# Kernel tuning notes

Measured on AMD Instinct MI355X. Metric: run time of the kernel, lower is better.

## Reference

```python
import jax, jax.numpy as jnp
import numpy as np

DG = 8   # deformable groups
K = 3    # DCNv2 kernel size


def conv1x1(x, w):
    return jnp.einsum('bhwc,cf->bhwf', x, w)


def conv3x3_same(x, w, b):
    out = jax.lax.conv_general_dilated(x, w, (1, 1), 'SAME',
                                       dimension_numbers=('NHWC', 'HWIO', 'NHWC'))
    return out + b


def dcn_v2(x, offset, mask, weight, bias):
    # x: [B,H,W,C]; offset: [B,H,W,DG,K*K,2] (dy,dx); mask: [B,H,W,DG,K*K]
    B, H, W, C = x.shape
    cpg = C // DG
    ky, kx = jnp.meshgrid(jnp.arange(K) - (K // 2), jnp.arange(K) - (K // 2), indexing='ij')
    ky = ky.reshape(-1).astype(x.dtype)  # [K*K]
    kx = kx.reshape(-1).astype(x.dtype)
    iy = jnp.arange(H, dtype=x.dtype)[None, :, None, None, None]
    ix = jnp.arange(W, dtype=x.dtype)[None, None, :, None, None]
    yp = iy + ky + offset[..., 0]   # [B,H,W,DG,KK] sample rows
    xp = ix + kx + offset[..., 1]   # sample cols

    # group-major flattened feature map for gather: [B,DG,H*W,cpg]
    xt = jnp.transpose(x.reshape(B, H, W, DG, cpg), (0, 3, 1, 2, 4)).reshape(B, DG, H * W, cpg)

    def gather(yi, xi):
        valid = ((yi >= 0) & (yi < H) & (xi >= 0) & (xi < W)).astype(x.dtype)
        yc = jnp.clip(yi, 0, H - 1)
        xc = jnp.clip(xi, 0, W - 1)
        flat = (yc * W + xc).astype(jnp.int32)               # [B,H,W,DG,KK]
        idx = jnp.transpose(flat, (0, 3, 1, 2, 4)).reshape(B, DG, -1)
        v = jnp.take_along_axis(xt, idx[..., None], axis=2)  # [B,DG,H*W*KK,cpg]
        v = v.reshape(B, DG, H, W, K * K, cpg)
        v = jnp.transpose(v, (0, 2, 3, 1, 4, 5))             # [B,H,W,DG,KK,cpg]
        return v * valid[..., None]

    y0 = jnp.floor(yp); x0 = jnp.floor(xp)
    wy = (yp - y0)[..., None]; wx = (xp - x0)[..., None]
    val = (gather(y0, x0) * (1 - wy) * (1 - wx)
           + gather(y0, x0 + 1) * (1 - wy) * wx
           + gather(y0 + 1, x0) * wy * (1 - wx)
           + gather(y0 + 1, x0 + 1) * wy * wx)
    val = val * mask[..., None]                               # modulated sampling
    # [B,H,W,DG,KK,cpg] -> [B,H,W,KK,C] (global channel = g*cpg + r)
    val = jnp.transpose(val, (0, 1, 2, 4, 3, 5)).reshape(B, H, W, K * K, C)
    out = jnp.einsum('bhwkc,kcf->bhwf', val, weight.reshape(K * K, C, -1))
    return out + bias


def setup_inputs() -> dict:
    key = jax.random.key(0)
    ks = jax.random.split(key, 8)
    B, H, W, Cf, Cc, F = 4, 64, 64, 256, 256, 256
    fine = jax.random.normal(ks[0], (B, H, W, Cf), jnp.float32)
    coarse = jax.random.normal(ks[1], (B, H // 2, W // 2, Cc), jnp.float32)
    attend_w = jax.random.normal(ks[2], (Cf, Cf), jnp.float32) * 0.05
    select_w = jax.random.normal(ks[3], (Cf, F), jnp.float32) * 0.05
    offset_w = jax.random.normal(ks[4], (F + Cc, 2 * F), jnp.float32) * 0.05
    om_w = jax.random.normal(ks[5], (3, 3, 2 * F, DG * 3 * K * K), jnp.float32) * 0.01
    om_b = jnp.zeros((DG * 3 * K * K,), jnp.float32)
    dcn_w = jax.random.normal(ks[6], (3, 3, Cc, F), jnp.float32) * 0.05
    dcn_b = jnp.zeros((F,), jnp.float32)
    return {'fine': fine, 'coarse': coarse, 'attend_w': attend_w, 'select_w': select_w,
            'offset_w': offset_w, 'om_w': om_w, 'om_b': om_b, 'dcn_w': dcn_w, 'dcn_b': dcn_b}


def reference(fine, coarse, attend_w, select_w, offset_w, om_w, om_b, dcn_w, dcn_b):
    B, H, W, Cf = fine.shape
    Cc = coarse.shape[-1]
    # BilinearInterpolation: upsample coarse to fine resolution
    coarse_up = jax.image.resize(coarse, (B, H, W, Cc), 'bilinear')
    # FeatureSelection: GAP -> 1x1 sigmoid attention, residual gate, 1x1 proj
    attn = jax.nn.sigmoid(conv1x1(jnp.mean(fine, axis=(1, 2), keepdims=True), attend_w))
    fine_cal = conv1x1(fine * (attn + 1.0), select_w)
    # offset features from concat(selected fine, 2*coarse)
    align = conv1x1(jnp.concatenate([fine_cal, coarse_up * 2.0], axis=-1), offset_w)
    # DCNv2 internal offset/mask conv (3x3) on alignment features
    om = conv3x3_same(align, om_w, om_b)          # [B,H,W,DG*3*K*K]
    n_off = DG * 2 * K * K
    off = om[..., :n_off].reshape(B, H, W, DG, K * K, 2)
    mask = jax.nn.sigmoid(om[..., n_off:]).reshape(B, H, W, DG, K * K)
    aligned = dcn_v2(coarse_up, off, mask, dcn_w, dcn_b)
    return jax.nn.relu(aligned) + fine_cal
```

## Files before the change

kernel.cpp:

```cpp
#include <hip/hip_runtime.h>
#include <math.h>


typedef __attribute__((ext_vector_type(8))) short bf16x8;
typedef __attribute__((ext_vector_type(4))) short bf16x4;
typedef __attribute__((ext_vector_type(4))) float f32x4;
#define MFMA16(a,b,c) __builtin_amdgcn_mfma_f32_16x16x32_bf16(a,b,c,0,0,0)

__device__ inline short f2b(float x){
  union { float f; unsigned u; } v; v.f = x;
  unsigned r = v.u + 0x7FFFu + ((v.u >> 16) & 1u);
  return (short)(r >> 16);
}
__device__ inline float b2f(short s){
  union { unsigned u; float f; } v;
  v.u = ((unsigned)(unsigned short)s) << 16;
  return v.f;
}

#define OFS_GATE  1024u
#define OFS_PART  2048u
#define OFS_CUPB  264192u
#define OFS_FCAL  4458496u
#define OFS_ALGB  8652800u
#define OFS_OM    12847104u
#define OFS_DWB   16386048u
#define OFS_OMWB  16680960u
#define OFS_SWB   17270784u
#define OFS_OWB   17401856u

__global__ __launch_bounds__(256) void k_gap(const float* __restrict__ fine,
                                             float* __restrict__ part){
  __shared__ float red[4*256];
  int b = blockIdx.x >> 6, chunk = blockIdx.x & 63;
  int c4 = threadIdx.x & 63, rl = threadIdx.x >> 6;
  const float4* F4 = (const float4*)fine;
  float4 s = {0.f,0.f,0.f,0.f};
  for (int it = 0; it < 16; ++it){
    int row = chunk*64 + it*4 + rl;
    float4 v = F4[((size_t)(b*4096 + row))*64 + c4];
    s.x += v.x; s.y += v.y; s.z += v.z; s.w += v.w;
  }
  *(float4*)&red[rl*256 + c4*4] = s;
  __syncthreads();
  int c = threadIdx.x;
  part[(size_t)blockIdx.x*256 + c] = red[c] + red[256+c] + red[512+c] + red[768+c];
}

__global__ __launch_bounds__(256) void k_misc(const float* __restrict__ part,
                                              const float* __restrict__ aw,
                                              float* __restrict__ gate,
                                              const float* __restrict__ dw,
                                              const float* __restrict__ omw,
                                              const float* __restrict__ ow,
                                              const float* __restrict__ sw,
                                              short* __restrict__ dwb,
                                              short* __restrict__ omwb,
                                              short* __restrict__ owb,
                                              short* __restrict__ swb,
                                              const float* __restrict__ coarse,
                                              short* __restrict__ cupb){
  int blk = blockIdx.x;
  if (blk < 4){
    __shared__ float m[256];
    int b = blk, f = threadIdx.x;
    float sm = 0.f;
    for (int ch = 0; ch < 64; ++ch) sm += part[(size_t)(b*64 + ch)*256 + f];
    m[f] = sm * (1.f/4096.f);
    __syncthreads();
    float s = 0.f;
    for (int c = 0; c < 256; ++c) s += m[c] * aw[c*256 + f];
    gate[b*256 + f] = 1.f + 1.f/(1.f + expf(-s));
  } else if (blk < 292){
    int t = (blk - 4)*256 + threadIdx.x;
    int l = t & 63, nt = (t >> 6) & 15, ksg = t >> 10;
    int n = nt*16 + (l & 15);
    int kb = ksg*32 + (l >> 4)*8;
    bf16x8 o;
#pragma unroll
    for (int j = 0; j < 8; ++j) o[j] = f2b(dw[(size_t)(kb + j)*256 + n]);
    ((bf16x8*)dwb)[t] = o;
  } else if (blk < 868){
    int t = (blk - 292)*256 + threadIdx.x;
    int l = t & 63, nt = (t >> 6) & 15, ksg = t >> 10;
    int n = nt*16 + (l & 15);
    int kb = ksg*32 + (l >> 4)*8;
    bf16x8 o;
#pragma unroll
    for (int j = 0; j < 8; ++j)
      o[j] = (n < 216) ? f2b(omw[(size_t)(kb + j)*216 + n]) : (short)0;
    ((bf16x8*)omwb)[t] = o;
  } else if (blk < 996){
    int t = (blk - 868)*256 + threadIdx.x;
    int l = t & 63, nt = (t >> 6) & 31, ksg = t >> 11;
    int n = nt*16 + (l & 15);
    int kb = ksg*32 + (l >> 4)*8;
    float sc = (kb >= 256) ? 2.f : 1.f;
    bf16x8 o;
#pragma unroll
    for (int j = 0; j < 8; ++j) o[j] = f2b(sc * ow[(size_t)(kb + j)*512 + n]);
    ((bf16x8*)owb)[t] = o;
  } else if (blk < 1124){
    int t = (blk - 996)*256 + threadIdx.x;
    int l = t & 63, nt = (t >> 6) & 15, ksg = t >> 10;
    int n = nt*16 + (l & 15);
    int kb = ksg*32 + (l >> 4)*8;
    bf16x8 o;
#pragma unroll
    for (int j = 0; j < 8; ++j) o[j] = f2b(sw[(size_t)(kb + j)*256 + n]);
    ((bf16x8*)swb)[t] = o;
  } else {
    int idx = (blk - 1124)*256 + threadIdx.x;
    int c4 = idx & 63, x = (idx >> 6) & 63, y = (idx >> 12) & 63, b = idx >> 18;
    float fy = 0.5f*y - 0.25f, fx = 0.5f*x - 0.25f;
    float yf = floorf(fy), xf = floorf(fx);
    float wy = fy - yf, wx = fx - xf;
    int r0 = max(0, min(31, (int)yf)), r1 = max(0, min(31, (int)yf + 1));
    int c0 = max(0, min(31, (int)xf)), c1 = max(0, min(31, (int)xf + 1));
    const float4* src = (const float4*)coarse;
    float4 v00 = src[((b*32 + r0)*32 + c0)*64 + c4];
    float4 v01 = src[((b*32 + r0)*32 + c1)*64 + c4];
    float4 v10 = src[((b*32 + r1)*32 + c0)*64 + c4];
    float4 v11 = src[((b*32 + r1)*32 + c1)*64 + c4];
    float w00 = (1.f-wy)*(1.f-wx), w01 = (1.f-wy)*wx, w10 = wy*(1.f-wx), w11 = wy*wx;
    bf16x4 o = { f2b(v00.x*w00 + v01.x*w01 + v10.x*w10 + v11.x*w11),
                 f2b(v00.y*w00 + v01.y*w01 + v10.y*w10 + v11.y*w11),
                 f2b(v00.z*w00 + v01.z*w01 + v10.z*w10 + v11.z*w11),
                 f2b(v00.w*w00 + v01.w*w01 + v10.w*w10 + v11.w*w11) };
    ((bf16x4*)cupb)[idx] = o;
  }
}

#define FST 264
__global__ __launch_bounds__(512) void k_fa(const float* __restrict__ fine,
                                            const float* __restrict__ gate,
                                            const short* __restrict__ swb,
                                            const short* __restrict__ owb,
                                            const short* __restrict__ cupb,
                                            float* __restrict__ fcal,
                                            short* __restrict__ algb){
  __shared__ float g4[256];
  __shared__ short ab[32*FST];
  int bid = ((blockIdx.x & 7) << 6) | (blockIdx.x >> 3);
  int m0 = bid*32, b = m0 >> 12;
  int tid = threadIdx.x, lane = tid & 63, wave = tid >> 6;
  int arow = lane & 15, aquad = lane >> 4;
  if (tid < 256) g4[tid] = gate[b*256 + tid];
  __syncthreads();
  const float4* F4 = (const float4*)(fine + (size_t)m0*256);
  const float4* G4 = (const float4*)g4;
  for (int it = 0; it < 4; ++it){
    int idx = it*512 + tid;
    int row = idx >> 6, c4 = idx & 63;
    float4 v = F4[row*64 + c4];
    float4 gg = G4[c4];
    bf16x4 s4 = { f2b(v.x*gg.x), f2b(v.y*gg.y), f2b(v.z*gg.z), f2b(v.w*gg.w) };
    *(bf16x4*)&ab[row*FST + c4*4] = s4;
  }
  __syncthreads();
  f32x4 acc[2][2];
#pragma unroll
  for (int s = 0; s < 2; ++s)
#pragma unroll
    for (int t = 0; t < 2; ++t) acc[s][t] = (f32x4){0.f,0.f,0.f,0.f};
  const bf16x8* W8 = (const bf16x8*)swb;
  for (int ks = 0; ks < 8; ++ks){
    bf16x8 a0 = *(const bf16x8*)&ab[arow*FST + ks*32 + aquad*8];
    bf16x8 a1 = *(const bf16x8*)&ab[(16 + arow)*FST + ks*32 + aquad*8];
    const bf16x8* wp = W8 + ((size_t)(ks*16 + wave*2))*64 + lane;
#pragma unroll
    for (int t = 0; t < 2; ++t){
      bf16x8 bw = wp[t*64];
      acc[0][t] = MFMA16(a0, bw, acc[0][t]);
      acc[1][t] = MFMA16(a1, bw, acc[1][t]);
    }
  }
  __syncthreads();
#pragma unroll
  for (int t = 0; t < 2; ++t){
    int f = wave*32 + t*16 + arow;
#pragma unroll
    for (int s = 0; s < 2; ++s)
#pragma unroll
      for (int r = 0; r < 4; ++r){
        int mloc = s*16 + aquad*4 + r;
        float v = acc[s][t][r];
        fcal[(size_t)(m0 + mloc)*256 + f] = v;
        ab[mloc*FST + f] = f2b(v);
      }
  }
  __syncthreads();
  f32x4 acc2[2][4];
#pragma unroll
  for (int s = 0; s < 2; ++s)
#pragma unroll
    for (int t = 0; t < 4; ++t) acc2[s][t] = (f32x4){0.f,0.f,0.f,0.f};
  const bf16x8* OW8 = (const bf16x8*)owb;
  for (int ks = 0; ks < 16; ++ks){
    bf16x8 a0, a1;
    if (ks < 8){
      a0 = *(const bf16x8*)&ab[arow*FST + ks*32 + aquad*8];
      a1 = *(const bf16x8*)&ab[(16 + arow)*FST + ks*32 + aquad*8];
    } else {
      int ko = (ks - 8)*32 + aquad*8;
      a0 = *(const bf16x8*)(cupb + (size_t)(m0 + arow)*256 + ko);
      a1 = *(const bf16x8*)(cupb + (size_t)(m0 + 16 + arow)*256 + ko);
    }
    const bf16x8* wp = OW8 + ((size_t)(ks*32 + wave*4))*64 + lane;
#pragma unroll
    for (int t = 0; t < 4; ++t){
      bf16x8 bw = wp[t*64];
      acc2[0][t] = MFMA16(a0, bw, acc2[0][t]);
      acc2[1][t] = MFMA16(a1, bw, acc2[1][t]);
    }
  }
#pragma unroll
  for (int t = 0; t < 4; ++t){
    int n = wave*64 + t*16 + arow;
#pragma unroll
    for (int s = 0; s < 2; ++s)
#pragma unroll
      for (int r = 0; r < 4; ++r){
        int m = m0 + s*16 + aquad*4 + r;
        algb[(size_t)m*512 + n] = f2b(acc2[s][t][r]);
      }
  }
}

#define XST2 264
__global__ __launch_bounds__(512) void k_om(const short* __restrict__ algb,
                                            const short* __restrict__ omwb,
                                            const float* __restrict__ omb,
                                            float* __restrict__ om){
  __shared__ short xbuf[66*XST2];
  int blk = ((blockIdx.x & 7) << 5) | (blockIdx.x >> 3);
  int m0 = blk*64;
  int b = m0 >> 12, y = (m0 >> 6) & 63;
  int tid = threadIdx.x;
  int lane = tid & 63, wave = tid >> 6;
  int arow = lane & 15, aquad = lane >> 4;
  f32x4 acc[4][2];
#pragma unroll
  for (int mi = 0; mi < 4; ++mi)
#pragma unroll
    for (int t = 0; t < 2; ++t) acc[mi][t] = (f32x4){0.f,0.f,0.f,0.f};
  const bf16x8* W8 = (const bf16x8*)omwb;
  for (int ky = 0; ky < 3; ++ky){
    int yy = y + ky - 1;
    if ((unsigned)yy >= 64u) continue;
    const short* srow = algb + (size_t)((b*64 + yy)*64)*512;
    for (int h = 0; h < 2; ++h){
      __syncthreads();
      for (int it = 0; it < 5; ++it){
        int u = it*512 + tid;
        if (u < 2112){
          int xx = u >> 5, cu = u & 31;
          int gx = xx - 1;
          bf16x8 v = (bf16x8){0,0,0,0,0,0,0,0};
          if ((unsigned)gx < 64u)
            v = *(const bf16x8*)(srow + (size_t)gx*512 + h*256 + cu*8);
          *(bf16x8*)&xbuf[xx*XST2 + cu*8] = v;
        }
      }
      __syncthreads();
#pragma unroll
      for (int kx = 0; kx < 3; ++kx){
        for (int s = 0; s < 8; ++s){
          int w48 = kx*16 + h*8 + s;
          bf16x8 a[4];
#pragma unroll
          for (int mi = 0; mi < 4; ++mi)
            a[mi] = *(const bf16x8*)&xbuf[(mi*16 + arow + kx)*XST2 + s*32 + aquad*8];
          const bf16x8* wp = W8 + ((size_t)((ky*48 + w48)*16 + wave*2))*64 + lane;
#pragma unroll
          for (int t = 0; t < 2; ++t){
            bf16x8 bw = wp[t*64];
#pragma unroll
            for (int mi = 0; mi < 4; ++mi)
              acc[mi][t] = MFMA16(a[mi], bw, acc[mi][t]);
          }
        }
      }
    }
  }
#pragma unroll
  for (int t = 0; t < 2; ++t){
    int f = wave*32 + t*16 + arow;
    if (f < 216){
      float bias = omb[f];
      bool is_mask = (f >= 144);
#pragma unroll
      for (int mi = 0; mi < 4; ++mi)
#pragma unroll
        for (int r = 0; r < 4; ++r){
          int m = m0 + mi*16 + aquad*4 + r;
          float v = acc[mi][t][r] + bias;
          if (is_mask) v = 1.f/(1.f + expf(-v));
          om[(size_t)m*216 + f] = v;
        }
    }
  }
}

#define VST 776
__global__ __launch_bounds__(512) void k_dcn(const short* __restrict__ cupb,
                                             const float* __restrict__ om,
                                             const short* __restrict__ dwb,
                                             const float* __restrict__ db,
                                             const float* __restrict__ fcal,
                                             float* __restrict__ out){
  __shared__ short valb[32*VST];
  int bid = ((blockIdx.x & 7) << 6) | (blockIdx.x >> 3);
  int m0 = bid*32;
  int b = m0 >> 12, y = (m0 & 4095) >> 6, x0 = m0 & 63;
  int tid = threadIdx.x;
  int lane = tid & 63, wave = tid >> 6;
  int unit = tid >> 2, lane4 = tid & 3;
  int arow = lane & 15, aquad = lane >> 4;
  f32x4 acc[2][2];
#pragma unroll
  for (int s = 0; s < 2; ++s)
#pragma unroll
    for (int t = 0; t < 2; ++t) acc[s][t] = (f32x4){0.f,0.f,0.f,0.f};
  const short* cpb = cupb + (size_t)b*4096*256;
  const bf16x8* W8 = (const bf16x8*)dwb;

  for (int ph = 0; ph < 3; ++ph){
    __syncthreads();
    for (int it = 0; it < 6; ++it){
      int u = it*128 + unit;
      int i = u / 24; int r = u - i*24; int g = r / 3; int kk = r - g*3;
      const float* omp = om + (size_t)(m0 + i)*216;
      int k = ph*3 + kk;
      float dy = omp[(g*9 + k)*2 + 0];
      float dx = omp[(g*9 + k)*2 + 1];
      float mv = omp[144 + g*9 + k];
      float yp = (float)(y + ph - 1) + dy;
      float xp = (float)(x0 + i + kk - 1) + dx;
      float yf = floorf(yp), xf = floorf(xp);
      float wy = yp - yf, wx = xp - xf;
      int iy = (int)yf, ix = (int)xf;
      float wA = (1.f-wy)*(1.f-wx), wB = (1.f-wy)*wx, wC = wy*(1.f-wx), wD = wy*wx;
      bool y0ok = (unsigned)iy < 64u, y1ok = (unsigned)(iy+1) < 64u;
      bool x0ok = (unsigned)ix < 64u, x1ok = (unsigned)(ix+1) < 64u;
      if (!(y0ok && x0ok)) wA = 0.f;
      if (!(y0ok && x1ok)) wB = 0.f;
      if (!(y1ok && x0ok)) wC = 0.f;
      if (!(y1ok && x1ok)) wD = 0.f;
      int y0c = min(max(iy, 0), 63), y1c = min(max(iy + 1, 0), 63);
      int x0c = min(max(ix, 0), 63), x1c = min(max(ix + 1, 0), 63);
      int cofs = g*32 + lane4*8;
      bf16x8 l00 = *(const bf16x8*)(cpb + (size_t)(y0c*64 + x0c)*256 + cofs);
      bf16x8 l01 = *(const bf16x8*)(cpb + (size_t)(y0c*64 + x1c)*256 + cofs);
      bf16x8 l10 = *(const bf16x8*)(cpb + (size_t)(y1c*64 + x0c)*256 + cofs);
      bf16x8 l11 = *(const bf16x8*)(cpb + (size_t)(y1c*64 + x1c)*256 + cofs);
      bf16x8 o;
#pragma unroll
      for (int j = 0; j < 8; ++j){
        float v = wA*b2f(l00[j]) + wB*b2f(l01[j]) + wC*b2f(l10[j]) + wD*b2f(l11[j]);
        o[j] = f2b(v * mv);
      }
      *(bf16x8*)&valb[i*VST + kk*256 + g*32 + lane4*8] = o;
    }
    __syncthreads();
    for (int ks = 0; ks < 24; ++ks){
      bf16x8 a0 = *(const bf16x8*)&valb[arow*VST + ks*32 + aquad*8];
      bf16x8 a1 = *(const bf16x8*)&valb[(16 + arow)*VST + ks*32 + aquad*8];
      const bf16x8* wp = W8 + ((size_t)((ph*24 + ks)*16 + wave*2))*64 + lane;
#pragma unroll
      for (int t = 0; t < 2; ++t){
        bf16x8 bw = wp[t*64];
        acc[0][t] = MFMA16(a0, bw, acc[0][t]);
        acc[1][t] = MFMA16(a1, bw, acc[1][t]);
      }
    }
  }
#pragma unroll
  for (int t = 0; t < 2; ++t){
    int f = wave*32 + t*16 + (lane & 15);
    float bias = db[f];
#pragma unroll
    for (int s = 0; s < 2; ++s)
#pragma unroll
      for (int r = 0; r < 4; ++r){
        int m = m0 + s*16 + aquad*4 + r;
        out[(size_t)m*256 + f] = fmaxf(acc[s][t][r] + bias, 0.f) + fcal[(size_t)m*256 + f];
      }
  }
}

extern "C" void kernel_launch(void* const* d_in, const int* in_sizes, int n_in,
                              void* d_out, int out_size, void* d_ws, size_t ws_size,
                              hipStream_t stream){
  const float* fine     = (const float*)d_in[0];
  const float* coarse   = (const float*)d_in[1];
  const float* attend_w = (const float*)d_in[2];
  const float* select_w = (const float*)d_in[3];
  const float* offset_w = (const float*)d_in[4];
  const float* om_w     = (const float*)d_in[5];
  const float* om_b     = (const float*)d_in[6];
  const float* dcn_w    = (const float*)d_in[7];
  const float* dcn_b    = (const float*)d_in[8];
  float* out = (float*)d_out;
  float* ws  = (float*)d_ws;

  float* gate = ws + OFS_GATE;
  float* part = ws + OFS_PART;
  short* cupb = (short*)(ws + OFS_CUPB);
  float* fcal = ws + OFS_FCAL;
  short* algb = (short*)(ws + OFS_ALGB);
  float* om   = ws + OFS_OM;
  short* dwb  = (short*)(ws + OFS_DWB);
  short* omwb = (short*)(ws + OFS_OMWB);
  short* swb  = (short*)(ws + OFS_SWB);
  short* owb  = (short*)(ws + OFS_OWB);

  hipLaunchKernelGGL(k_gap,  dim3(256),  dim3(256), 0, stream, fine, part);
  hipLaunchKernelGGL(k_misc, dim3(5220), dim3(256), 0, stream, part, attend_w, gate,
                     dcn_w, om_w, offset_w, select_w, dwb, omwb, owb, swb, coarse, cupb);
  hipLaunchKernelGGL(k_fa,   dim3(512),  dim3(512), 0, stream, fine, gate, swb, owb,
                     cupb, fcal, algb);
  hipLaunchKernelGGL(k_om,   dim3(256),  dim3(512), 0, stream, algb, omwb, om_b, om);
  hipLaunchKernelGGL(k_dcn,  dim3(512),  dim3(512), 0, stream, cupb, om, dwb, dcn_b, fcal, out);
  (void)in_sizes; (void)n_in; (void)out_size; (void)ws_size;
}
```

Baseline: 222.0 us.

## Split-K the 3x3 offset conv across wave groups with LDS reduction

The k_om kernel now stages the full 512-channel row into shared memory once per ky instead of two 256-channel halves, which halves the number of barriers and staging passes. The 8 waves are regrouped into 2 K-groups × 4 N-groups, with each wave computing 64 output columns over half the channels. The two partial sums are then reduced through LDS before the bias/sigmoid epilogue. This doubles accumulator registers per wave and roughly doubles shared memory use, which may lower occupancy, and it adds a reduction barrier.

```diff
diff --git a/kernel.cpp b/kernel.cpp
--- a/kernel.cpp
+++ b/kernel.cpp
@@ -227,77 +227,91 @@
   }
 }
 
-#define XST2 264
+#define XST3 520
 __global__ __launch_bounds__(512) void k_om(const short* __restrict__ algb,
                                             const short* __restrict__ omwb,
                                             const float* __restrict__ omb,
                                             float* __restrict__ om){
-  __shared__ short xbuf[66*XST2];
+  __shared__ short xbuf[66*XST3];
   int blk = ((blockIdx.x & 7) << 5) | (blockIdx.x >> 3);
   int m0 = blk*64;
   int b = m0 >> 12, y = (m0 >> 6) & 63;
   int tid = threadIdx.x;
   int lane = tid & 63, wave = tid >> 6;
+  int kg = wave >> 2, ng = wave & 3;
   int arow = lane & 15, aquad = lane >> 4;
-  f32x4 acc[4][2];
+  f32x4 acc[4][4];
 #pragma unroll
   for (int mi = 0; mi < 4; ++mi)
 #pragma unroll
-    for (int t = 0; t < 2; ++t) acc[mi][t] = (f32x4){0.f,0.f,0.f,0.f};
+    for (int t = 0; t < 4; ++t) acc[mi][t] = (f32x4){0.f,0.f,0.f,0.f};
   const bf16x8* W8 = (const bf16x8*)omwb;
   for (int ky = 0; ky < 3; ++ky){
     int yy = y + ky - 1;
     if ((unsigned)yy >= 64u) continue;
     const short* srow = algb + (size_t)((b*64 + yy)*64)*512;
-    for (int h = 0; h < 2; ++h){
-      __syncthreads();
-      for (int it = 0; it < 5; ++it){
-        int u = it*512 + tid;
-        if (u < 2112){
-          int xx = u >> 5, cu = u & 31;
-          int gx = xx - 1;
-          bf16x8 v = (bf16x8){0,0,0,0,0,0,0,0};
-          if ((unsigned)gx < 64u)
-            v = *(const bf16x8*)(srow + (size_t)gx*512 + h*256 + cu*8);
-          *(bf16x8*)&xbuf[xx*XST2 + cu*8] = v;
+    __syncthreads();
+    for (int it = 0; it < 9; ++it){
+      int u = it*512 + tid;
+      if (u < 4224){
+        int xx = u >> 6, cu = u & 63;
+        int gx = xx - 1;
+        bf16x8 v = (bf16x8){0,0,0,0,0,0,0,0};
+        if ((unsigned)gx < 64u)
+          v = *(const bf16x8*)(srow + (size_t)gx*512 + cu*8);
+        *(bf16x8*)&xbuf[xx*XST3 + cu*8] = v;
+      }
+    }
+    __syncthreads();
+#pragma unroll
+    for (int kx = 0; kx < 3; ++kx){
+      for (int s = 0; s < 8; ++s){
+        int ksg = ky*48 + kx*16 + kg*8 + s;
+        bf16x8 a[4];
+#pragma unroll
+        for (int mi = 0; mi < 4; ++mi)
+          a[mi] = *(const bf16x8*)&xbuf[(mi*16 + arow + kx)*XST3 + kg*256 + s*32 + aquad*8];
+        const bf16x8* wp = W8 + ((size_t)(ksg*16 + ng*4))*64 + lane;
+#pragma unroll
+        for (int t = 0; t < 4; ++t){
+          bf16x8 bw = wp[t*64];
+#pragma unroll
+          for (int mi = 0; mi < 4; ++mi)
+            acc[mi][t] = MFMA16(a[mi], bw, acc[mi][t]);
         }
       }
-      __syncthreads();
-#pragma unroll
-      for (int kx = 0; kx < 3; ++kx){
-        for (int s = 0; s < 8; ++s){
-          int w48 = kx*16 + h*8 + s;
-          bf16x8 a[4];
-#pragma unroll
-          for (int mi = 0; mi < 4; ++mi)
-            a[mi] = *(const bf16x8*)&xbuf[(mi*16 + arow + kx)*XST2 + s*32 + aquad*8];
-          const bf16x8* wp = W8 + ((size_t)((ky*48 + w48)*16 + wave*2))*64 + lane;
-#pragma unroll
-          for (int t = 0; t < 2; ++t){
-            bf16x8 bw = wp[t*64];
-#pragma unroll
-            for (int mi = 0; mi < 4; ++mi)
-              acc[mi][t] = MFMA16(a[mi], bw, acc[mi][t]);
+    }
+  }
+  __syncthreads();
+  f32x4* sc = (f32x4*)xbuf;
+  if (kg == 1){
+#pragma unroll
+    for (int mi = 0; mi < 4; ++mi)
+#pragma unroll
+      for (int t = 0; t < 4; ++t)
+        sc[(mi*4 + t)*256 + ng*64 + lane] = acc[mi][t];
+  }
+  __syncthreads();
+  if (kg == 0){
+#pragma unroll
+    for (int t = 0; t < 4; ++t){
+      int f = ng*64 + t*16 + arow;
+      bool valid = (f < 216);
+      float bias = valid ? omb[f] : 0.f;
+      bool is_mask = (f >= 144);
+#pragma unroll
+      for (int mi = 0; mi < 4; ++mi){
+        f32x4 other = sc[(mi*4 + t)*256 + ng*64 + lane];
+        if (valid){
+#pragma unroll
+          for (int r = 0; r < 4; ++r){
+            int m = m0 + mi*16 + aquad*4 + r;
+            float v = acc[mi][t][r] + other[r] + bias;
+            if (is_mask) v = 1.f/(1.f + expf(-v));
+            om[(size_t)m*216 + f] = v;
           }
         }
       }
-    }
-  }
-#pragma unroll
-  for (int t = 0; t < 2; ++t){
-    int f = wave*32 + t*16 + arow;
-    if (f < 216){
-      float bias = omb[f];
-      bool is_mask = (f >= 144);
-#pragma unroll
-      for (int mi = 0; mi < 4; ++mi)
-#pragma unroll
-        for (int r = 0; r < 4; ++r){
-          int m = m0 + mi*16 + aquad*4 + r;
-          float v = acc[mi][t][r] + bias;
-          if (is_mask) v = 1.f/(1.f + expf(-v));
-          om[(size_t)m*216 + f] = v;
-        }
     }
   }
 }
```

Measured after the change: 267.6 us. 1.21x slower.
